# Optimization experiments

Hardware: AMD Instinct MI355X
Metric: run time of the kernel (lower is better)

Reference implementation:

```python
import jax, jax.numpy as jnp
import numpy as np

SIGMA = 1.0  # Gaussian perturbation scale


def setup_inputs() -> dict:
    key = jax.random.key(0)
    k1, k2, k3 = jax.random.split(key, 3)
    S, B, D = 64, 128, 10000
    theta = jax.random.normal(k1, (B, D), dtype=jnp.float32)
    y = jax.random.uniform(k2, (B, D), dtype=jnp.float32)
    noise = jax.random.normal(k3, (S, B, D), dtype=jnp.float32)  # eta = theta + SIGMA*noise
    return {"theta": theta, "y": y, "noise": noise}


def reference(theta, y, noise):
    # eta = ptb.sample(theta, samples=S): [S, B, D]
    eta = theta[None, :, :] + SIGMA * noise
    # oracle.call vectorized over (S, B): softmax over feature dim
    pi = jax.nn.softmax(eta, axis=-1)  # [S, B, D]
    # loss(pi[i], y) -> per-example vector [B]: MSE mean over features
    losses = jnp.mean((pi - y[None, :, :]) ** 2, axis=-1)  # [S, B]
    # val = losses.mean(dim=(0, 1)) -> scalar
    val = jnp.mean(losses)
    return val
```

## Files before the change

kernel.cpp:

```cpp
#include <hip/hip_runtime.h>

#define S_DIM 64
#define B_DIM 128
#define D_DIM 10000
#define NV4   2500
#define BLOCK 512
#define RPB   8
#define NBLK  (B_DIM * (S_DIM / RPB))
#define NROWS (S_DIM * B_DIM)
#define NWAVE (BLOCK / 64)
#define FULLIT 39

static __device__ __forceinline__ unsigned bf16pack(float lo, float hi) {
    unsigned a = __builtin_bit_cast(unsigned, lo);
    unsigned b = __builtin_bit_cast(unsigned, hi);
    a = (a + 0x7fffu + ((a >> 16) & 1u)) >> 16;
    b = (b + 0x7fffu + ((b >> 16) & 1u)) & 0xffff0000u;
    return (a & 0xffffu) | b;
}
static __device__ __forceinline__ float bf16lo(unsigned u) {
    return __builtin_bit_cast(float, u << 16);
}
static __device__ __forceinline__ float bf16hi(unsigned u) {
    return __builtin_bit_cast(float, u & 0xffff0000u);
}

__global__ __launch_bounds__(BLOCK, 8) void perturbed_loss_waverow(
    const float* __restrict__ theta,
    const float* __restrict__ y,
    const float* __restrict__ noise,
    double* __restrict__ blockloss,
    float*  __restrict__ y2arr)
{
    __shared__ uint4  TV[NV4];
    __shared__ float  redY[NWAVE];
    __shared__ double wloss[NWAVE];

    const int blk  = blockIdx.x;
    const int b    = ((blk >> 6) << 3) + (blk & 7);
    const int s0   = ((blk >> 3) & 7) * RPB;
    const int tid  = threadIdx.x;
    const int lane = tid & 63;
    const int wave = tid >> 6;

    const float4* th4 = reinterpret_cast<const float4*>(theta + (size_t)b * D_DIM);
    const float4* y4  = reinterpret_cast<const float4*>(y     + (size_t)b * D_DIM);

    float y2 = 0.0f;
    for (int i = tid; i < NV4; i += BLOCK) {
        float4 t  = th4[i];
        float4 yy = y4[i];
        unsigned tp0 = bf16pack(__expf(t.x), __expf(t.y));
        unsigned tp1 = bf16pack(__expf(t.z), __expf(t.w));
        unsigned wp0 = bf16pack(bf16lo(tp0) * yy.x, bf16hi(tp0) * yy.y);
        unsigned wp1 = bf16pack(bf16lo(tp1) * yy.z, bf16hi(tp1) * yy.w);
        TV[i] = make_uint4(tp0, tp1, wp0, wp1);
        y2 = fmaf(yy.x, yy.x, y2); y2 = fmaf(yy.y, yy.y, y2);
        y2 = fmaf(yy.z, yy.z, y2); y2 = fmaf(yy.w, yy.w, y2);
    }
    #pragma unroll
    for (int o = 32; o > 0; o >>= 1) y2 += __shfl_down(y2, o, 64);
    if (lane == 0) redY[wave] = y2;
    __syncthreads();
    if (tid == 0 && ((blk >> 3) & 7) == 0) {
        float t = 0.0f;
        #pragma unroll
        for (int w = 0; w < NWAVE; ++w) t += redY[w];
        y2arr[b] = t;
    }

    const int row = (s0 + wave) * B_DIM + b;
    const float4* nz4 = reinterpret_cast<const float4*>(noise + (size_t)row * D_DIM);

    float s = 0.0f, q = 0.0f, p = 0.0f;
    int i = lane;
    #pragma unroll 4
    for (int it = 0; it < FULLIT; ++it, i += 64) {
        float4 n = nz4[i];
        uint4  u = TV[i];
        float e0 = __expf(n.x), e1 = __expf(n.y);
        float e2 = __expf(n.z), e3 = __expf(n.w);
        float t0 = bf16lo(u.x) * e0, t1 = bf16hi(u.x) * e1;
        float t2 = bf16lo(u.y) * e2, t3 = bf16hi(u.y) * e3;
        s += (t0 + t1) + (t2 + t3);
        q = fmaf(t0, t0, q); q = fmaf(t1, t1, q);
        q = fmaf(t2, t2, q); q = fmaf(t3, t3, q);
        p = fmaf(bf16lo(u.z), e0, p); p = fmaf(bf16hi(u.z), e1, p);
        p = fmaf(bf16lo(u.w), e2, p); p = fmaf(bf16hi(u.w), e3, p);
    }
    if (lane < 4) {
        const int j = FULLIT * 64 + lane;
        float4 n = nz4[j];
        uint4  u = TV[j];
        float e0 = __expf(n.x), e1 = __expf(n.y);
        float e2 = __expf(n.z), e3 = __expf(n.w);
        float t0 = bf16lo(u.x) * e0, t1 = bf16hi(u.x) * e1;
        float t2 = bf16lo(u.y) * e2, t3 = bf16hi(u.y) * e3;
        s += (t0 + t1) + (t2 + t3);
        q = fmaf(t0, t0, q); q = fmaf(t1, t1, q);
        q = fmaf(t2, t2, q); q = fmaf(t3, t3, q);
        p = fmaf(bf16lo(u.z), e0, p); p = fmaf(bf16hi(u.z), e1, p);
        p = fmaf(bf16lo(u.w), e2, p); p = fmaf(bf16hi(u.w), e3, p);
    }
    #pragma unroll
    for (int o = 32; o > 0; o >>= 1) {
        s += __shfl_down(s, o, 64);
        q += __shfl_down(q, o, 64);
        p += __shfl_down(p, o, 64);
    }
    if (lane == 0) {
        double invS = 1.0 / (double)s;
        wloss[wave] = ((double)q * invS - 2.0 * (double)p) * invS;
    }
    __syncthreads();
    if (tid == 0) {
        double t = 0.0;
        #pragma unroll
        for (int w = 0; w < NWAVE; ++w) t += wloss[w];
        blockloss[blk] = t;
    }
}

__global__ __launch_bounds__(256) void reduce_final(
    const double* __restrict__ blockloss,
    const float*  __restrict__ y2arr,
    float* __restrict__ out)
{
    __shared__ double red[4];
    const int tid  = threadIdx.x;
    const int lane = tid & 63;
    const int wave = tid >> 6;

    double acc = 0.0;
    for (int i = tid; i < NBLK; i += 256) acc += blockloss[i];
    if (tid < B_DIM) acc += (double)S_DIM * (double)y2arr[tid];
    #pragma unroll
    for (int o = 32; o > 0; o >>= 1) acc += __shfl_down(acc, o, 64);
    if (lane == 0) red[wave] = acc;
    __syncthreads();
    if (tid == 0) {
        double t = ((red[0] + red[1]) + (red[2] + red[3]));
        out[0] = (float)(t / ((double)S_DIM * (double)B_DIM * (double)D_DIM));
    }
}

extern "C" void kernel_launch(void* const* d_in, const int* in_sizes, int n_in,
                              void* d_out, int out_size, void* d_ws, size_t ws_size,
                              hipStream_t stream) {
    const float* theta = (const float*)d_in[0];
    const float* y     = (const float*)d_in[1];
    const float* noise = (const float*)d_in[2];
    float* out        = (float*)d_out;
    double* blockloss = (double*)d_ws;
    float*  y2arr     = (float*)((char*)d_ws + NBLK * sizeof(double));

    perturbed_loss_waverow<<<NBLK, BLOCK, 0, stream>>>(theta, y, noise,
                                                       blockloss, y2arr);
    reduce_final<<<1, 256, 0, stream>>>(blockloss, y2arr, out);
}
```

Before: 67.66 us.

## Fuse final reduction via last-block atomic counter and use nontemporal noise loads

Drops the separate single-block reduce kernel. Each block now bumps an atomic counter, and the last block to finish does the final sum and writes the output. Noise loads become nontemporal so the streamed data does not pollute the cache. This saves a kernel launch gap but adds a memset node and an atomic per block, and the y2arr write relies on the acq_rel ordering to be visible.

```diff
diff --git a/kernel.cpp b/kernel.cpp
--- a/kernel.cpp
+++ b/kernel.cpp
@@ -10,6 +10,8 @@
 #define NROWS (S_DIM * B_DIM)
 #define NWAVE (BLOCK / 64)
 #define FULLIT 39
+
+typedef float floatx4 __attribute__((ext_vector_type(4)));
 
 static __device__ __forceinline__ unsigned bf16pack(float lo, float hi) {
     unsigned a = __builtin_bit_cast(unsigned, lo);
@@ -30,11 +32,15 @@
     const float* __restrict__ y,
     const float* __restrict__ noise,
     double* __restrict__ blockloss,
-    float*  __restrict__ y2arr)
+    float*  __restrict__ y2arr,
+    unsigned int* __restrict__ counter,
+    float* __restrict__ out)
 {
     __shared__ uint4  TV[NV4];
     __shared__ float  redY[NWAVE];
     __shared__ double wloss[NWAVE];
+    __shared__ double dred[NWAVE];
+    __shared__ int    is_last;
 
     const int blk  = blockIdx.x;
     const int b    = ((blk >> 6) << 3) + (blk & 7);
@@ -70,13 +76,13 @@
     }
 
     const int row = (s0 + wave) * B_DIM + b;
-    const float4* nz4 = reinterpret_cast<const float4*>(noise + (size_t)row * D_DIM);
+    const floatx4* nz4 = reinterpret_cast<const floatx4*>(noise + (size_t)row * D_DIM);
 
     float s = 0.0f, q = 0.0f, p = 0.0f;
     int i = lane;
     #pragma unroll 4
     for (int it = 0; it < FULLIT; ++it, i += 64) {
-        float4 n = nz4[i];
+        floatx4 n = __builtin_nontemporal_load(&nz4[i]);
         uint4  u = TV[i];
         float e0 = __expf(n.x), e1 = __expf(n.y);
         float e2 = __expf(n.z), e3 = __expf(n.w);
@@ -90,7 +96,7 @@
     }
     if (lane < 4) {
         const int j = FULLIT * 64 + lane;
-        float4 n = nz4[j];
+        floatx4 n = __builtin_nontemporal_load(&nz4[j]);
         uint4  u = TV[j];
         float e0 = __expf(n.x), e1 = __expf(n.y);
         float e2 = __expf(n.z), e3 = __expf(n.w);
@@ -113,34 +119,36 @@
         wloss[wave] = ((double)q * invS - 2.0 * (double)p) * invS;
     }
     __syncthreads();
+
     if (tid == 0) {
         double t = 0.0;
         #pragma unroll
         for (int w = 0; w < NWAVE; ++w) t += wloss[w];
         blockloss[blk] = t;
+        unsigned int old = __hip_atomic_fetch_add(counter, 1u, __ATOMIC_ACQ_REL,
+                                                  __HIP_MEMORY_SCOPE_AGENT);
+        is_last = (old == (unsigned int)(NBLK - 1)) ? 1 : 0;
     }
-}
-
-__global__ __launch_bounds__(256) void reduce_final(
-    const double* __restrict__ blockloss,
-    const float*  __restrict__ y2arr,
-    float* __restrict__ out)
-{
-    __shared__ double red[4];
-    const int tid  = threadIdx.x;
-    const int lane = tid & 63;
-    const int wave = tid >> 6;
-
-    double acc = 0.0;
-    for (int i = tid; i < NBLK; i += 256) acc += blockloss[i];
-    if (tid < B_DIM) acc += (double)S_DIM * (double)y2arr[tid];
-    #pragma unroll
-    for (int o = 32; o > 0; o >>= 1) acc += __shfl_down(acc, o, 64);
-    if (lane == 0) red[wave] = acc;
     __syncthreads();
-    if (tid == 0) {
-        double t = ((red[0] + red[1]) + (red[2] + red[3]));
-        out[0] = (float)(t / ((double)S_DIM * (double)B_DIM * (double)D_DIM));
+    if (is_last) {
+        double acc = 0.0;
+        for (int i2 = tid; i2 < NBLK; i2 += BLOCK)
+            acc += __hip_atomic_load(&blockloss[i2], __ATOMIC_RELAXED,
+                                     __HIP_MEMORY_SCOPE_AGENT);
+        if (tid < B_DIM)
+            acc += (double)S_DIM *
+                   (double)__hip_atomic_load(&y2arr[tid], __ATOMIC_RELAXED,
+                                             __HIP_MEMORY_SCOPE_AGENT);
+        #pragma unroll
+        for (int o = 32; o > 0; o >>= 1) acc += __shfl_down(acc, o, 64);
+        if (lane == 0) dred[wave] = acc;
+        __syncthreads();
+        if (tid == 0) {
+            double t = 0.0;
+            #pragma unroll
+            for (int w = 0; w < NWAVE; ++w) t += dred[w];
+            out[0] = (float)(t / ((double)S_DIM * (double)B_DIM * (double)D_DIM));
+        }
     }
 }
 
@@ -153,8 +161,11 @@
     float* out        = (float*)d_out;
     double* blockloss = (double*)d_ws;
     float*  y2arr     = (float*)((char*)d_ws + NBLK * sizeof(double));
+    unsigned int* counter =
+        (unsigned int*)((char*)d_ws + NBLK * sizeof(double) + 512);
 
+    (void)hipMemsetAsync(counter, 0, sizeof(unsigned int), stream);
     perturbed_loss_waverow<<<NBLK, BLOCK, 0, stream>>>(theta, y, noise,
-                                                       blockloss, y2arr);
-    reduce_final<<<1, 256, 0, stream>>>(blockloss, y2arr, out);
+                                                       blockloss, y2arr,
+                                                       counter, out);
 }
```

Measured after the change: 109.7 us. 62.1% more time.
